# Kernel optimization log

Measured on AMD Instinct MI355X. Metric: run time of the kernel, lower is better.

Reference implementation:

```python
import jax, jax.numpy as jnp
import numpy as np

N_NODES = 100000
N_EDGES = 1250000
IN_DIM = 128
HID_DIM = 64
OUT_DIM = 16


def setup_inputs() -> dict:
    key = jax.random.key(0)
    k1, k2, k3, k4, k5, k6, k7 = jax.random.split(key, 7)
    x = jax.random.normal(k1, (N_NODES, IN_DIM), dtype=jnp.float32)
    edge_index = jax.random.randint(k2, (2, N_EDGES), 0, N_NODES, dtype=jnp.int64)
    s = 1.0 / np.sqrt(IN_DIM)
    W1 = jax.random.uniform(k3, (IN_DIM, HID_DIM), jnp.float32, -s, s)
    b1 = jax.random.uniform(k4, (HID_DIM,), jnp.float32, -s, s)
    s2 = 1.0 / np.sqrt(HID_DIM)
    W2 = jax.random.uniform(k5, (HID_DIM, OUT_DIM), jnp.float32, -s2, s2)
    b2 = jax.random.uniform(k6, (OUT_DIM,), jnp.float32, -s2, s2)
    return {"x": x, "edge_index": edge_index, "W1": W1, "b1": b1, "W2": W2, "b2": b2}


def reference(x, edge_index, W1, b1, W2, b2):
    # GCNConv (PyG default): linear transform, add self-loops, symmetric norm,
    # gather-scatter aggregation, bias. Then relu -> linear -> log_softmax.
    N = x.shape[0]
    loop = jnp.arange(N, dtype=edge_index.dtype)
    src = jnp.concatenate([edge_index[0], loop])  # message sources
    dst = jnpp_concat = jnp.concatenate([edge_index[1], loop])  # message targets
    # degree (with self-loops) computed on destination nodes
    deg = jax.ops.segment_sum(jnp.ones_like(dst, dtype=x.dtype), dst, num_segments=N)
    deg_inv_sqrt = jnp.where(deg > 0, jax.lax.rsqrt(deg), 0.0)
    norm = deg_inv_sqrt[src] * deg_inv_sqrt[dst]  # [E+N]
    h = x @ W1  # [N, hid] -- transform before aggregation (fewer bytes moved)
    msg = h[src] * norm[:, None]  # gather: [E+N, hid]
    agg = jax.ops.segment_sum(msg, dst, num_segments=N) + b1  # scatter-add
    h = jax.nn.relu(agg)
    logits = h @ W2 + b2
    return jax.nn.log_softmax(logits, axis=-1)
```

## Files before the change

### kernel.cpp

```cpp
#include <hip/hip_runtime.h>
#include <hip/hip_bf16.h>

#define N_NODES 100000
#define N_EDGES 1250000
#define IN_DIM  128
#define HID     64
#define OUTD    16
#define ROW     64
#define NRANGE  8
#define RSIZE   12500
#define NCHUNK  128
#define CHUNK   9768
#define FILLB   (NRANGE * NCHUNK)
#define MTILE   128
#define GEMMB   ((N_NODES + MTILE - 1) / MTILE)

typedef __attribute__((ext_vector_type(8))) short  short8;
typedef __attribute__((ext_vector_type(4))) float  floatx4;
typedef __attribute__((ext_vector_type(4))) float  f32x4;
typedef __attribute__((ext_vector_type(4))) int    i32x4;

__device__ __forceinline__ unsigned short f2bf(float f) {
    unsigned u = __float_as_uint(f);
    u += 0x7fffu + ((u >> 16) & 1u);
    return (unsigned short)(u >> 16);
}
__device__ __forceinline__ unsigned pk2(float lo, float hi) {
    __hip_bfloat162 t = __float22bfloat162_rn(make_float2(lo, hi));
    return *reinterpret_cast<unsigned*>(&t);
}
__device__ __forceinline__ float bf2f_lo(unsigned u) { return __uint_as_float(u << 16); }
__device__ __forceinline__ float bf2f_hi(unsigned u) { return __uint_as_float(u & 0xffff0000u); }

__global__ __launch_bounds__(256) void fill_gemm(const float* __restrict__ x,
                                                 const float* __restrict__ W1,
                                                 const int* __restrict__ src,
                                                 const int* __restrict__ dst,
                                                 int* __restrict__ cursor,
                                                 int* __restrict__ csr,
                                                 unsigned short* __restrict__ hb) {
    __shared__ unsigned short w1t[HID][132];

    if (blockIdx.x < FILLB) {
        const int r  = blockIdx.x & 7;
        const int c  = blockIdx.x >> 3;
        const int lo = r * RSIZE;
        const int q1 = min(N_EDGES, (c + 1) * CHUNK) >> 2;
        for (int q = (c * CHUNK >> 2) + threadIdx.x; q < q1; q += 256) {
            i32x4 d4 = __builtin_nontemporal_load(((const i32x4*)dst) + q);
            i32x4 s4 = __builtin_nontemporal_load(((const i32x4*)src) + q);
#pragma unroll
            for (int u = 0; u < 4; u++) {
                int d = (u == 0) ? d4.x : (u == 1) ? d4.y : (u == 2) ? d4.z : d4.w;
                int s = (u == 0) ? s4.x : (u == 1) ? s4.y : (u == 2) ? s4.z : s4.w;
                if ((unsigned)(d - lo) < (unsigned)RSIZE) {
                    int p = atomicAdd(&cursor[d], 1);
                    if (p < ROW) csr[(size_t)d * ROW + p] = s;
                }
            }
        }
        return;
    }

    const int m0 = (blockIdx.x - FILLB) * MTILE;

    for (int q = threadIdx.x; q < IN_DIM * HID / 4; q += 256) {
        int k = q >> 4, n = (q & 15) * 4;
        float4 wq = ((const float4*)W1)[q];
        w1t[n + 0][k] = f2bf(wq.x);
        w1t[n + 1][k] = f2bf(wq.y);
        w1t[n + 2][k] = f2bf(wq.z);
        w1t[n + 3][k] = f2bf(wq.w);
    }
    __syncthreads();

    const int lane = threadIdx.x & 63;
    const int w    = threadIdx.x >> 6;
    const int mrow = lane & 15;
    const int quad = lane >> 4;
    const int rowa = min(m0 + w * 32 + mrow,      N_NODES - 1);
    const int rowb = min(m0 + w * 32 + 16 + mrow, N_NODES - 1);

    floatx4 acc[2][4] = {};
#pragma unroll
    for (int k0 = 0; k0 < IN_DIM; k0 += 32) {
        union { unsigned u[4]; short8 s; } a0, a1;
        {
            const f32x4* pa = (const f32x4*)(x + (size_t)rowa * IN_DIM + k0 + quad * 8);
            f32x4 u0 = __builtin_nontemporal_load(pa);
            f32x4 v0 = __builtin_nontemporal_load(pa + 1);
            a0.u[0] = pk2(u0.x, u0.y); a0.u[1] = pk2(u0.z, u0.w);
            a0.u[2] = pk2(v0.x, v0.y); a0.u[3] = pk2(v0.z, v0.w);
            const f32x4* pb = (const f32x4*)(x + (size_t)rowb * IN_DIM + k0 + quad * 8);
            f32x4 u1 = __builtin_nontemporal_load(pb);
            f32x4 v1 = __builtin_nontemporal_load(pb + 1);
            a1.u[0] = pk2(u1.x, u1.y); a1.u[1] = pk2(u1.z, u1.w);
            a1.u[2] = pk2(v1.x, v1.y); a1.u[3] = pk2(v1.z, v1.w);
        }
        short8 b0 = *(const short8*)&w1t[ 0 + mrow][k0 + quad * 8];
        short8 b1 = *(const short8*)&w1t[16 + mrow][k0 + quad * 8];
        short8 b2 = *(const short8*)&w1t[32 + mrow][k0 + quad * 8];
        short8 b3 = *(const short8*)&w1t[48 + mrow][k0 + quad * 8];
        acc[0][0] = __builtin_amdgcn_mfma_f32_16x16x32_bf16(a0.s, b0, acc[0][0], 0, 0, 0);
        acc[0][1] = __builtin_amdgcn_mfma_f32_16x16x32_bf16(a0.s, b1, acc[0][1], 0, 0, 0);
        acc[0][2] = __builtin_amdgcn_mfma_f32_16x16x32_bf16(a0.s, b2, acc[0][2], 0, 0, 0);
        acc[0][3] = __builtin_amdgcn_mfma_f32_16x16x32_bf16(a0.s, b3, acc[0][3], 0, 0, 0);
        acc[1][0] = __builtin_amdgcn_mfma_f32_16x16x32_bf16(a1.s, b0, acc[1][0], 0, 0, 0);
        acc[1][1] = __builtin_amdgcn_mfma_f32_16x16x32_bf16(a1.s, b1, acc[1][1], 0, 0, 0);
        acc[1][2] = __builtin_amdgcn_mfma_f32_16x16x32_bf16(a1.s, b2, acc[1][2], 0, 0, 0);
        acc[1][3] = __builtin_amdgcn_mfma_f32_16x16x32_bf16(a1.s, b3, acc[1][3], 0, 0, 0);
    }

#pragma unroll
    for (int tm = 0; tm < 2; tm++) {
#pragma unroll
        for (int reg = 0; reg < 4; reg++) {
            int m = m0 + w * 32 + tm * 16 + quad * 4 + reg;
            if (m < N_NODES) {
#pragma unroll
                for (int tn = 0; tn < 4; tn++)
                    __builtin_nontemporal_store(f2bf(acc[tm][tn][reg]),
                                                &hb[(size_t)m * HID + tn * 16 + mrow]);
            }
        }
    }
}

__global__ __launch_bounds__(256) void pull_epilogue(const unsigned short* __restrict__ hb,
                                                     const int* __restrict__ csr,
                                                     const int* __restrict__ deg,
                                                     const float* __restrict__ b1,
                                                     const float* __restrict__ W2,
                                                     const float* __restrict__ b2,
                                                     float* __restrict__ out) {
    const int lane  = threadIdx.x & 63;
    const int e_sub = lane >> 4;
    const int f4    = lane & 15;
    const int iA    = blockIdx.x * 8 + (threadIdx.x >> 6) * 2;
    const int iB    = iA + 1;

    const int   dgA  = deg[iA],               dgB  = deg[iB];
    const int   cntA = min(dgA, ROW - 1),     cntB = min(dgB, ROW - 1);
    const float diA  = rsqrtf((float)dgA + 1.0f);
    const float diB  = rsqrtf((float)dgB + 1.0f);

    int   sA = N_NODES, sB = N_NODES;
    if (lane < cntA) sA = __builtin_nontemporal_load(csr + (size_t)iA * ROW + lane);
    if (lane < cntB) sB = __builtin_nontemporal_load(csr + (size_t)iB * ROW + lane);
    float wA = 0.f, wB = 0.f;
    if (lane < cntA)       wA = rsqrtf((float)deg[sA] + 1.0f);
    else if (lane == cntA) { sA = iA; wA = diA; }
    if (lane < cntB)       wB = rsqrtf((float)deg[sB] + 1.0f);
    else if (lane == cntB) { sB = iB; wB = diB; }

    const uint2* hbv = (const uint2*)hb + f4;

    float axA = 0.f, ayA = 0.f, azA = 0.f, awA = 0.f;
    float axB = 0.f, ayB = 0.f, azB = 0.f, awB = 0.f;
    const int RA = (cntA + 16) >> 4, RB = (cntB + 16) >> 4;
    const int R  = max(RA, RB);
    for (int r = 0; r < R; ++r) {
        const int e0 = (r << 4) + e_sub;
        if (r < RA) {
            int   s0 = __shfl(sA, e0,      64), s1 = __shfl(sA, e0 + 4,  64);
            int   s2 = __shfl(sA, e0 + 8,  64), s3 = __shfl(sA, e0 + 12, 64);
            float w0 = __shfl(wA, e0,      64), w1 = __shfl(wA, e0 + 4,  64);
            float w2 = __shfl(wA, e0 + 8,  64), w3 = __shfl(wA, e0 + 12, 64);
            uint2 a = hbv[s0 << 4];
            uint2 b = hbv[s1 << 4];
            uint2 c = hbv[s2 << 4];
            uint2 d = hbv[s3 << 4];
            axA = fmaf(bf2f_lo(a.x), w0, axA); ayA = fmaf(bf2f_hi(a.x), w0, ayA);
            azA = fmaf(bf2f_lo(a.y), w0, azA); awA = fmaf(bf2f_hi(a.y), w0, awA);
            axA = fmaf(bf2f_lo(b.x), w1, axA); ayA = fmaf(bf2f_hi(b.x), w1, ayA);
            azA = fmaf(bf2f_lo(b.y), w1, azA); awA = fmaf(bf2f_hi(b.y), w1, awA);
            axA = fmaf(bf2f_lo(c.x), w2, axA); ayA = fmaf(bf2f_hi(c.x), w2, ayA);
            azA = fmaf(bf2f_lo(c.y), w2, azA); awA = fmaf(bf2f_hi(c.y), w2, awA);
            axA = fmaf(bf2f_lo(d.x), w3, axA); ayA = fmaf(bf2f_hi(d.x), w3, ayA);
            azA = fmaf(bf2f_lo(d.y), w3, azA); awA = fmaf(bf2f_hi(d.y), w3, awA);
        }
        if (r < RB) {
            int   s0 = __shfl(sB, e0,      64), s1 = __shfl(sB, e0 + 4,  64);
            int   s2 = __shfl(sB, e0 + 8,  64), s3 = __shfl(sB, e0 + 12, 64);
            float w0 = __shfl(wB, e0,      64), w1 = __shfl(wB, e0 + 4,  64);
            float w2 = __shfl(wB, e0 + 8,  64), w3 = __shfl(wB, e0 + 12, 64);
            uint2 a = hbv[s0 << 4];
            uint2 b = hbv[s1 << 4];
            uint2 c = hbv[s2 << 4];
            uint2 d = hbv[s3 << 4];
            axB = fmaf(bf2f_lo(a.x), w0, axB); ayB = fmaf(bf2f_hi(a.x), w0, ayB);
            azB = fmaf(bf2f_lo(a.y), w0, azB); awB = fmaf(bf2f_hi(a.y), w0, awB);
            axB = fmaf(bf2f_lo(b.x), w1, axB); ayB = fmaf(bf2f_hi(b.x), w1, ayB);
            azB = fmaf(bf2f_lo(b.y), w1, azB); awB = fmaf(bf2f_hi(b.y), w1, awB);
            axB = fmaf(bf2f_lo(c.x), w2, axB); ayB = fmaf(bf2f_hi(c.x), w2, ayB);
            azB = fmaf(bf2f_lo(c.y), w2, azB); awB = fmaf(bf2f_hi(c.y), w2, awB);
            axB = fmaf(bf2f_lo(d.x), w3, axB); ayB = fmaf(bf2f_hi(d.x), w3, ayB);
            azB = fmaf(bf2f_lo(d.y), w3, azB); awB = fmaf(bf2f_hi(d.y), w3, awB);
        }
    }

    axA += __shfl_xor(axA, 16, 64); axB += __shfl_xor(axB, 16, 64);
    ayA += __shfl_xor(ayA, 16, 64); ayB += __shfl_xor(ayB, 16, 64);
    azA += __shfl_xor(azA, 16, 64); azB += __shfl_xor(azB, 16, 64);
    awA += __shfl_xor(awA, 16, 64); awB += __shfl_xor(awB, 16, 64);
    axA += __shfl_xor(axA, 32, 64); axB += __shfl_xor(axB, 32, 64);
    ayA += __shfl_xor(ayA, 32, 64); ayB += __shfl_xor(ayB, 32, 64);
    azA += __shfl_xor(azA, 32, 64); azB += __shfl_xor(azB, 32, 64);
    awA += __shfl_xor(awA, 32, 64); awB += __shfl_xor(awB, 32, 64);

    float4 b1v = ((const float4*)b1)[f4];
    float v0A = fmaxf(fmaf(axA, diA, b1v.x), 0.f), v0B = fmaxf(fmaf(axB, diB, b1v.x), 0.f);
    float v1A = fmaxf(fmaf(ayA, diA, b1v.y), 0.f), v1B = fmaxf(fmaf(ayB, diB, b1v.y), 0.f);
    float v2A = fmaxf(fmaf(azA, diA, b1v.z), 0.f), v2B = fmaxf(fmaf(azB, diB, b1v.z), 0.f);
    float v3A = fmaxf(fmaf(awA, diA, b1v.w), 0.f), v3B = fmaxf(fmaf(awB, diB, b1v.w), 0.f);

    const float4* W2v = (const float4*)W2;
    float4 w2r0 = W2v[(4 * f4 + 0) * 4 + e_sub];
    float4 w2r1 = W2v[(4 * f4 + 1) * 4 + e_sub];
    float4 w2r2 = W2v[(4 * f4 + 2) * 4 + e_sub];
    float4 w2r3 = W2v[(4 * f4 + 3) * 4 + e_sub];
    float p0A = v0A * w2r0.x + v1A * w2r1.x + v2A * w2r2.x + v3A * w2r3.x;
    float p1A = v0A * w2r0.y + v1A * w2r1.y + v2A * w2r2.y + v3A * w2r3.y;
    float p2A = v0A * w2r0.z + v1A * w2r1.z + v2A * w2r2.z + v3A * w2r3.z;
    float p3A = v0A * w2r0.w + v1A * w2r1.w + v2A * w2r2.w + v3A * w2r3.w;
    float p0B = v0B * w2r0.x + v1B * w2r1.x + v2B * w2r2.x + v3B * w2r3.x;
    float p1B = v0B * w2r0.y + v1B * w2r1.y + v2B * w2r2.y + v3B * w2r3.y;
    float p2B = v0B * w2r0.z + v1B * w2r1.z + v2B * w2r2.z + v3B * w2r3.z;
    float p3B = v0B * w2r0.w + v1B * w2r1.w + v2B * w2r2.w + v3B * w2r3.w;
#pragma unroll
    for (int d = 1; d < 16; d <<= 1) {
        p0A += __shfl_xor(p0A, d, 64); p0B += __shfl_xor(p0B, d, 64);
        p1A += __shfl_xor(p1A, d, 64); p1B += __shfl_xor(p1B, d, 64);
        p2A += __shfl_xor(p2A, d, 64); p2B += __shfl_xor(p2B, d, 64);
        p3A += __shfl_xor(p3A, d, 64); p3B += __shfl_xor(p3B, d, 64);
    }
    float4 b2v = ((const float4*)b2)[e_sub];
    float lg0A = p0A + b2v.x, lg1A = p1A + b2v.y, lg2A = p2A + b2v.z, lg3A = p3A + b2v.w;
    float lg0B = p0B + b2v.x, lg1B = p1B + b2v.y, lg2B = p2B + b2v.z, lg3B = p3B + b2v.w;

    float mA = fmaxf(fmaxf(lg0A, lg1A), fmaxf(lg2A, lg3A));
    float mB = fmaxf(fmaxf(lg0B, lg1B), fmaxf(lg2B, lg3B));
    mA = fmaxf(mA, __shfl_xor(mA, 16, 64)); mB = fmaxf(mB, __shfl_xor(mB, 16, 64));
    mA = fmaxf(mA, __shfl_xor(mA, 32, 64)); mB = fmaxf(mB, __shfl_xor(mB, 32, 64));
    float sA_ = __expf(lg0A - mA) + __expf(lg1A - mA) + __expf(lg2A - mA) + __expf(lg3A - mA);
    float sB_ = __expf(lg0B - mB) + __expf(lg1B - mB) + __expf(lg2B - mB) + __expf(lg3B - mB);
    sA_ += __shfl_xor(sA_, 16, 64); sB_ += __shfl_xor(sB_, 16, 64);
    sA_ += __shfl_xor(sA_, 32, 64); sB_ += __shfl_xor(sB_, 32, 64);
    float lseA = __logf(sA_) + mA;
    float lseB = __logf(sB_) + mB;

    if (f4 == 0) {
        f32x4 oA = {lg0A - lseA, lg1A - lseA, lg2A - lseA, lg3A - lseA};
        f32x4 oB = {lg0B - lseB, lg1B - lseB, lg2B - lseB, lg3B - lseB};
        __builtin_nontemporal_store(oA, ((f32x4*)out) + (size_t)iA * 4 + e_sub);
        __builtin_nontemporal_store(oB, ((f32x4*)out) + (size_t)iB * 4 + e_sub);
    }
}

extern "C" void kernel_launch(void* const* d_in, const int* in_sizes, int n_in,
                              void* d_out, int out_size, void* d_ws, size_t ws_size,
                              hipStream_t stream) {
    const float* x   = (const float*)d_in[0];
    const int*   ei  = (const int*)d_in[1];
    const float* W1  = (const float*)d_in[2];
    const float* b1  = (const float*)d_in[3];
    const float* W2  = (const float*)d_in[4];
    const float* b2  = (const float*)d_in[5];
    float*       out = (float*)d_out;

    const int* src = ei;
    const int* dst = ei + N_EDGES;

    char* ws = (char*)d_ws;
    size_t off = 0;
    unsigned short* hb = (unsigned short*)(ws + off);
    off += (size_t)(N_NODES + 1) * HID * 2;
    int*   csr    = (int*)  (ws + off); off += ((size_t)N_NODES * ROW + ROW) * 4;
    int*   cursor = (int*)  (ws + off); off += (size_t)N_NODES * 4;

    hipMemsetAsync(cursor, 0, (size_t)N_NODES * 4, stream);
    hipMemsetAsync(hb + (size_t)N_NODES * HID, 0, HID * sizeof(unsigned short), stream);

    fill_gemm<<<FILLB + GEMMB, 256, 0, stream>>>(x, W1, src, dst, cursor, csr, hb);
    pull_epilogue<<<N_NODES / 8, 256, 0, stream>>>(hb, csr, cursor, b1, W2, b2, out);
}
```

Before: 216.1 us.

## Batch edge loads and atomics in CSR fill; drop padding row memset

The CSR fill phase now uses smaller chunks (more blocks). Each thread issues all four vector loads of dst/src up front, then all 16 atomicAdds, then the stores. This raises memory-level parallelism and keeps atomics in flight instead of serialising load→atomic→store per element. The sentinel padding row in hb and its memset are removed, with out-of-range lanes now defaulting to source 0, which saves one launch and relies on the lane index staying unused.

```diff
diff --git a/kernel.cpp b/kernel.cpp
--- a/kernel.cpp
+++ b/kernel.cpp
@@ -9,8 +9,8 @@
 #define ROW     64
 #define NRANGE  8
 #define RSIZE   12500
-#define NCHUNK  128
-#define CHUNK   9768
+#define NCHUNK  306
+#define CHUNK   4096
 #define FILLB   (NRANGE * NCHUNK)
 #define MTILE   128
 #define GEMMB   ((N_NODES + MTILE - 1) / MTILE)
@@ -45,18 +45,40 @@
         const int r  = blockIdx.x & 7;
         const int c  = blockIdx.x >> 3;
         const int lo = r * RSIZE;
+        const int qb = (c * CHUNK >> 2) + threadIdx.x;
         const int q1 = min(N_EDGES, (c + 1) * CHUNK) >> 2;
-        for (int q = (c * CHUNK >> 2) + threadIdx.x; q < q1; q += 256) {
-            i32x4 d4 = __builtin_nontemporal_load(((const i32x4*)dst) + q);
-            i32x4 s4 = __builtin_nontemporal_load(((const i32x4*)src) + q);
+
+        i32x4 d[4], s[4];
+#pragma unroll
+        for (int j = 0; j < 4; j++) {
+            int q = qb + j * 256;
+            if (q < q1) {
+                d[j] = __builtin_nontemporal_load(((const i32x4*)dst) + q);
+                s[j] = __builtin_nontemporal_load(((const i32x4*)src) + q);
+            } else {
+                i32x4 neg = {-1, -1, -1, -1};
+                d[j] = neg; s[j] = neg;
+            }
+        }
+
+        int p[16];
+#pragma unroll
+        for (int j = 0; j < 4; j++) {
 #pragma unroll
             for (int u = 0; u < 4; u++) {
-                int d = (u == 0) ? d4.x : (u == 1) ? d4.y : (u == 2) ? d4.z : d4.w;
-                int s = (u == 0) ? s4.x : (u == 1) ? s4.y : (u == 2) ? s4.z : s4.w;
-                if ((unsigned)(d - lo) < (unsigned)RSIZE) {
-                    int p = atomicAdd(&cursor[d], 1);
-                    if (p < ROW) csr[(size_t)d * ROW + p] = s;
-                }
+                const int e = j * 4 + u;
+                p[e] = ROW;
+                const int dd = d[j][u];
+                if ((unsigned)(dd - lo) < (unsigned)RSIZE)
+                    p[e] = atomicAdd(&cursor[dd], 1);
+            }
+        }
+#pragma unroll
+        for (int j = 0; j < 4; j++) {
+#pragma unroll
+            for (int u = 0; u < 4; u++) {
+                const int e = j * 4 + u;
+                if (p[e] < ROW) csr[(size_t)d[j][u] * ROW + p[e]] = s[j][u];
             }
         }
         return;
@@ -144,7 +166,7 @@
     const float diA  = rsqrtf((float)dgA + 1.0f);
     const float diB  = rsqrtf((float)dgB + 1.0f);
 
-    int   sA = N_NODES, sB = N_NODES;
+    int   sA = 0, sB = 0;
     if (lane < cntA) sA = __builtin_nontemporal_load(csr + (size_t)iA * ROW + lane);
     if (lane < cntB) sB = __builtin_nontemporal_load(csr + (size_t)iB * ROW + lane);
     float wA = 0.f, wB = 0.f;
@@ -274,12 +296,11 @@
     char* ws = (char*)d_ws;
     size_t off = 0;
     unsigned short* hb = (unsigned short*)(ws + off);
-    off += (size_t)(N_NODES + 1) * HID * 2;
+    off += (size_t)N_NODES * HID * 2;
     int*   csr    = (int*)  (ws + off); off += ((size_t)N_NODES * ROW + ROW) * 4;
     int*   cursor = (int*)  (ws + off); off += (size_t)N_NODES * 4;
 
     hipMemsetAsync(cursor, 0, (size_t)N_NODES * 4, stream);
-    hipMemsetAsync(hb + (size_t)N_NODES * HID, 0, HID * sizeof(unsigned short), stream);
 
     fill_gemm<<<FILLB + GEMMB, 256, 0, stream>>>(x, W1, src, dst, cursor, csr, hb);
     pull_epilogue<<<N_NODES / 8, 256, 0, stream>>>(hb, csr, cursor, b1, W2, b2, out);
```

Measured after the change: 220.7 us. +2.1%, slower.
